# Kernel tuning notes

Hardware: AMD Instinct MI355X
Metric: run time of the kernel (lower is better)

The kernel has to match this reference:

```python
import jax, jax.numpy as jnp
import numpy as np

D_MODEL = 2048
NUM_HEADS = 16
D_HEAD = D_MODEL // NUM_HEADS


def setup_inputs() -> dict:
    key = jax.random.key(0)
    k_x, k_q, k_k, k_v, k_o, k_ob = jax.random.split(key, 6)
    B, L = 2, 2048
    s = 1.0 / np.sqrt(D_MODEL)
    return {
        "x": jax.random.normal(k_x, (B, L, D_MODEL), dtype=jnp.float32),
        # torch nn.Linear weights are (out_features, in_features)
        "Wq": jax.random.uniform(k_q, (D_MODEL, D_MODEL), jnp.float32, -s, s),
        "Wk": jax.random.uniform(k_k, (D_HEAD, D_MODEL), jnp.float32, -s, s),
        "Wv": jax.random.uniform(k_v, (D_HEAD, D_MODEL), jnp.float32, -s, s),
        "Wo": jax.random.uniform(k_o, (D_MODEL, D_MODEL), jnp.float32, -s, s),
        "bo": jax.random.uniform(k_ob, (D_MODEL,), jnp.float32, -s, s),
    }


def reference(x, Wq, Wk, Wv, Wo, bo):
    B, L, _ = x.shape
    H, dh = NUM_HEADS, D_HEAD
    Q = (x @ Wq.T).reshape(B, L, H, dh).transpose(0, 2, 1, 3)  # [B,H,L,dh]
    K = x @ Wk.T  # [B,L,dh] shared across heads (MQA)
    V = x @ Wv.T  # [B,L,dh]
    scores = jnp.einsum("bhqd,bkd->bhqk", Q, K) / np.sqrt(dh)  # [B,H,L,L]
    attn = jax.nn.softmax(scores, axis=-1)
    out = jnp.einsum("bhqk,bkd->bhqd", attn, V)  # [B,H,L,dh]
    out = out.transpose(0, 2, 1, 3).reshape(B, L, H * dh)
    return out @ Wo.T + bo
```

## Files before the change

### kernel.cpp

```cpp
#include <hip/hip_runtime.h>


typedef __attribute__((ext_vector_type(8))) short bf16x8;
typedef __attribute__((ext_vector_type(4))) short short4v;
typedef __attribute__((ext_vector_type(4))) float f32x4;
typedef __attribute__((ext_vector_type(16))) float f32x16;
typedef __attribute__((ext_vector_type(4))) int int4v;

__device__ __forceinline__ unsigned short f2bf(float f) {
  unsigned int u = __builtin_bit_cast(unsigned int, f);
  u += 0x7fffu + ((u >> 16) & 1u);
  return (unsigned short)(u >> 16);
}

__device__ __forceinline__ unsigned int cvtpk(float lo, float hi) {
  unsigned int r;
  asm("v_cvt_pk_bf16_f32 %0, %1, %2" : "=v"(r) : "v"(lo), "v"(hi));
  return r;
}

typedef __attribute__((address_space(1))) void gvoid_t;
typedef __attribute__((address_space(3))) void lvoid_t;

__device__ __forceinline__ void gll16(const void* g, void* l) {
  __builtin_amdgcn_global_load_lds((gvoid_t*)g, (lvoid_t*)l, 16, 0, 0);
}

__global__ void cast_all_kernel(
    const float* __restrict__ x, const float* __restrict__ wq,
    const float* __restrict__ wk, const float* __restrict__ wv,
    const float* __restrict__ wo, unsigned short* __restrict__ xb,
    unsigned short* __restrict__ wallb, unsigned short* __restrict__ wob) {
  const int NT = 4325376;
  int i = blockIdx.x * blockDim.x + threadIdx.x;
  const int stride = gridDim.x * blockDim.x;
  for (; i < NT; i += stride) {
    const float* src;
    unsigned short* dst;
    int j;
    if (i < 2097152) {
      src = x; dst = xb; j = i;
    } else if (i < 3145728) {
      src = wq; dst = wallb; j = i - 2097152;
    } else if (i < 3211264) {
      src = wk; dst = wallb + 2048 * 2048; j = i - 3145728;
    } else if (i < 3276800) {
      src = wv; dst = wallb + 2176 * 2048; j = i - 3211264;
    } else {
      src = wo; dst = wob; j = i - 3276800;
    }
    float4 f = reinterpret_cast<const float4*>(src)[j];
    short4v o;
    o.x = (short)f2bf(f.x);
    o.y = (short)f2bf(f.y);
    o.z = (short)f2bf(f.z);
    o.w = (short)f2bf(f.w);
    reinterpret_cast<short4v*>(dst)[j] = o;
  }
}

template <int MODE>
__global__ __launch_bounds__(256) void gemm_bt(
    const unsigned short* __restrict__ A, const unsigned short* __restrict__ B,
    void* __restrict__ Cout, int M, int N, int K, float scale,
    const float* __restrict__ bias, void* __restrict__ C2,
    void* __restrict__ C3) {
  __shared__ unsigned short As[128 * 64] __attribute__((aligned(16)));
  __shared__ unsigned short Bs[128 * 64] __attribute__((aligned(16)));

  const int tid = threadIdx.x;
  const int lane = tid & 63;
  const int wave = tid >> 6;
  const int lr = lane & 15;
  const int lg = lane >> 4;
  const int bm = blockIdx.x * 128;
  const int bn = blockIdx.y * 128;
  const int wrow = (wave >> 1) * 64;
  const int wcol = (wave & 1) * 64;

  f32x4 acc[4][4] = {};

  int soff[4];
#pragma unroll
  for (int t = 0; t < 4; t++) {
    int ci = t * 256 + tid;
    int row = ci >> 3;
    int c = (ci ^ row) & 7;
    soff[t] = row * K + c * 8;
  }
  const unsigned short* Abase = A + (size_t)bm * K;
  const unsigned short* Bbase = B + (size_t)bn * K;

  for (int k0 = 0; k0 < K; k0 += 64) {
    __syncthreads();
#pragma unroll
    for (int t = 0; t < 4; t++) {
      gll16(Abase + k0 + soff[t], (char*)As + (t * 256 + tid) * 16);
      gll16(Bbase + k0 + soff[t], (char*)Bs + (t * 256 + tid) * 16);
    }
    __syncthreads();

#pragma unroll
    for (int kh = 0; kh < 2; kh++) {
      bf16x8 af[4], bfr[4];
#pragma unroll
      for (int mi = 0; mi < 4; mi++) {
        const int row = wrow + mi * 16 + lr;
        const int ch = (lg + 4 * kh) ^ (row & 7);
        af[mi] = *(const bf16x8*)&As[row * 64 + ch * 8];
      }
#pragma unroll
      for (int nj = 0; nj < 4; nj++) {
        const int row = wcol + nj * 16 + lr;
        const int ch = (lg + 4 * kh) ^ (row & 7);
        bfr[nj] = *(const bf16x8*)&Bs[row * 64 + ch * 8];
      }
#pragma unroll
      for (int mi = 0; mi < 4; mi++)
#pragma unroll
        for (int nj = 0; nj < 4; nj++)
          acc[mi][nj] = __builtin_amdgcn_mfma_f32_16x16x32_bf16(
              af[mi], bfr[nj], acc[mi][nj], 0, 0, 0);
    }
  }

#pragma unroll
  for (int mi = 0; mi < 4; mi++)
#pragma unroll
    for (int nj = 0; nj < 4; nj++) {
      const int row = bm + wrow + mi * 16 + (lane >> 4) * 4;
      const int col = bn + wcol + nj * 16 + lr;
#pragma unroll
      for (int r = 0; r < 4; r++) {
        float v = acc[mi][nj][r];
        if constexpr (MODE == 2) {
          ((float*)Cout)[(size_t)(row + r) * N + col] = v + bias[col];
        } else {
          if (col < 2048)
            ((unsigned short*)Cout)[(size_t)(row + r) * 2048 + col] =
                f2bf(v * scale);
          else if (col < 2176)
            ((unsigned short*)C2)[(size_t)(row + r) * 128 + (col - 2048)] =
                f2bf(v);
          else
            ((unsigned short*)C3)[(size_t)(col - 2176) * M + (row + r)] =
                f2bf(v);
        }
      }
    }
}

__global__ __launch_bounds__(256, 3) void mqa_attn(
    const unsigned short* __restrict__ Q, const unsigned short* __restrict__ Kb,
    const unsigned short* __restrict__ VT, unsigned short* __restrict__ Ob) {
  __shared__ unsigned short Ksm[2][2][4096] __attribute__((aligned(16)));
  __shared__ unsigned short Vsm[2][4096] __attribute__((aligned(16)));
  __shared__ float mlbuf[2][32];

  const int tid = threadIdx.x;
  const int lane = tid & 63;
  const int wave = tid >> 6;
  const int grp = wave >> 1;
  const int wi = wave & 1;
  const int tg = tid & 127;
  const int l31 = lane & 31;
  const int hi = lane >> 5;
  const int bh = blockIdx.y;
  const int b = bh >> 4;
  const int h = bh & 15;
  const int q0 = blockIdx.x * 64 + wi * 32;
  const int kvbase = grp * 1024;

  const unsigned short* Qb = Q + ((size_t)(b * 2048 + q0)) * 2048 + h * 128;
  const unsigned short* Kbase = Kb + (size_t)b * 2048 * 128;
  const unsigned short* VTb = VT + (size_t)b * 2048;

  bf16x8 qf[8];
#pragma unroll
  for (int ks = 0; ks < 8; ks++)
    qf[ks] = *(const bf16x8*)&Qb[(size_t)l31 * 2048 + ks * 16 + hi * 8];

  f32x16 oacc[4] = {};
  float lrun = 0.0f;

  int koff[4], voff[4];
#pragma unroll
  for (int t = 0; t < 4; t++) {
    int ci = t * 128 + tg;
    int row = ci >> 4;
    int p = (ci ^ row) & 15;
    koff[t] = row * 128 + p * 8;
    voff[t] = (4 * row + (p >> 2)) * 4096 + (p & 3) * 8;
  }

  auto stageK = [&](int kv0, int bsel) {
    const unsigned short* kp = Kbase + (size_t)(kvbase + kv0) * 128;
    char* kb = (char*)&Ksm[grp][bsel][0];
#pragma unroll
    for (int t = 0; t < 4; t++) gll16(kp + koff[t], kb + (t * 128 + tg) * 16);
  };
  auto stageV = [&](int kv0) {
    const unsigned short* vp = VTb + kvbase + kv0;
    char* vb = (char*)&Vsm[grp][0];
#pragma unroll
    for (int t = 0; t < 4; t++) gll16(vp + voff[t], vb + (t * 128 + tg) * 16);
  };

  stageK(0, 0);
  stageV(0);
  asm volatile("s_waitcnt vmcnt(0)" ::: "memory");
  __builtin_amdgcn_sched_barrier(0);
  __builtin_amdgcn_s_barrier();

  for (int t = 0; t < 32; t++) {
    const int cur = t & 1;
    stageK(((t + 1) & 31) * 32, cur ^ 1);
    const unsigned short* Kt = &Ksm[grp][cur][0];
    const unsigned short* Vt = &Vsm[grp][0];

    f32x16 st = {};
#pragma unroll
    for (int ks = 0; ks < 8; ks++) {
      const int pos = (2 * ks + hi) ^ (l31 & 15);
      bf16x8 kf = *(const bf16x8*)&Kt[l31 * 128 + pos * 8];
      st = __builtin_amdgcn_mfma_f32_32x32x16_bf16(kf, qf[ks], st, 0, 0, 0);
    }

#pragma unroll
    for (int r = 0; r < 16; r++) st[r] = __builtin_amdgcn_exp2f(st[r]);
    {
      float s0 = (st[0] + st[1]) + (st[2] + st[3]);
      float s1 = (st[4] + st[5]) + (st[6] + st[7]);
      float s2 = (st[8] + st[9]) + (st[10] + st[11]);
      float s3 = (st[12] + st[13]) + (st[14] + st[15]);
      float ps = (s0 + s1) + (s2 + s3);
      lrun += ps + __shfl_xor(ps, 32);
    }

    bf16x8 paw[2];
#pragma unroll
    for (int h2 = 0; h2 < 2; h2++) {
      unsigned int a0 = cvtpk(st[8 * h2 + 0], st[8 * h2 + 1]);
      unsigned int a1 = cvtpk(st[8 * h2 + 2], st[8 * h2 + 3]);
      unsigned int b0 = cvtpk(st[8 * h2 + 4], st[8 * h2 + 5]);
      unsigned int b1 = cvtpk(st[8 * h2 + 6], st[8 * h2 + 7]);
      unsigned int s0 = hi ? a0 : b0;
      unsigned int s1 = hi ? a1 : b1;
      unsigned int r0 = (unsigned int)__shfl_xor((int)s0, 32);
      unsigned int r1 = (unsigned int)__shfl_xor((int)s1, 32);
      int4v w;
      w.x = (int)(hi ? r0 : a0);
      w.y = (int)(hi ? r1 : a1);
      w.z = (int)(hi ? b0 : r0);
      w.w = (int)(hi ? b1 : r1);
      paw[h2] = __builtin_bit_cast(bf16x8, w);
    }

    asm volatile("s_waitcnt vmcnt(4)" ::: "memory");
    __builtin_amdgcn_sched_barrier(0);
    __builtin_amdgcn_s_barrier();

#pragma unroll
    for (int dt = 0; dt < 4; dt++) {
      f32x16 z = oacc[dt];
      const int qr = dt * 8 + (l31 >> 2);
#pragma unroll
      for (int ks2 = 0; ks2 < 2; ks2++) {
        const int pos = (4 * (l31 & 3) + 2 * ks2 + hi) ^ (qr & 15);
        bf16x8 vfr = *(const bf16x8*)&Vt[qr * 128 + pos * 8];
        z = __builtin_amdgcn_mfma_f32_32x32x16_bf16(paw[ks2], vfr, z, 0, 0, 0);
      }
      oacc[dt] = z;
    }

    __builtin_amdgcn_s_barrier();
    stageV(((t + 1) & 31) * 32);
    asm volatile("s_waitcnt vmcnt(4)" ::: "memory");
    __builtin_amdgcn_sched_barrier(0);
    __builtin_amdgcn_s_barrier();
  }

  float* mg = (float*)&Ksm[0][0][0] + (size_t)wi * 4096;
  if (grp == 1) {
#pragma unroll
    for (int dt = 0; dt < 4; dt++)
#pragma unroll
      for (int r = 0; r < 16; r++)
        mg[(dt * 16 + r) * 64 + lane] = oacc[dt][r];
    if (hi == 0) mlbuf[wi][l31] = lrun;
  }
  __syncthreads();
  if (grp == 0) {
    float lb = mlbuf[wi][l31];
    float linv = 1.0f / (lrun + lb);
#pragma unroll
    for (int r = 0; r < 16; r++) {
      const int qrow = (r & 3) + 8 * (r >> 2) + 4 * hi;
      float invr = __shfl(linv, qrow);
      size_t row = (size_t)(b * 2048 + q0 + qrow);
#pragma unroll
      for (int dt = 0; dt < 4; dt++) {
        float o = (oacc[dt][r] + mg[(dt * 16 + r) * 64 + lane]) * invr;
        Ob[row * 2048 + h * 128 + dt * 32 + l31] = f2bf(o);
      }
    }
  }
}

extern "C" void kernel_launch(void* const* d_in, const int* in_sizes, int n_in,
                              void* d_out, int out_size, void* d_ws,
                              size_t ws_size, hipStream_t stream) {
  const float* x = (const float*)d_in[0];
  const float* Wq = (const float*)d_in[1];
  const float* Wk = (const float*)d_in[2];
  const float* Wv = (const float*)d_in[3];
  const float* Wo = (const float*)d_in[4];
  const float* bo = (const float*)d_in[5];

  const int Bb = 2, Lq = 2048, D = 2048, DH = 128;
  const int M = Bb * Lq;

  char* ws = (char*)d_ws;
  size_t off = 0;
  auto alloc = [&](size_t bytes) {
    void* p = ws + off;
    off += (bytes + 255) & ~size_t(255);
    return p;
  };
  unsigned short* x_bf = (unsigned short*)alloc((size_t)M * D * 2);
  unsigned short* Wall_bf = (unsigned short*)alloc((size_t)2304 * D * 2);
  unsigned short* Wo_bf = (unsigned short*)alloc((size_t)D * D * 2);
  unsigned short* Qbuf = (unsigned short*)alloc((size_t)M * D * 2);
  unsigned short* Kbuf = (unsigned short*)alloc((size_t)M * DH * 2);
  unsigned short* VTbuf = (unsigned short*)alloc((size_t)DH * M * 2);
  unsigned short* AObuf = (unsigned short*)alloc((size_t)M * D * 2);

  cast_all_kernel<<<2048, 256, 0, stream>>>(x, Wq, Wk, Wv, Wo, x_bf, Wall_bf,
                                            Wo_bf);

  gemm_bt<4><<<dim3(M / 128, 2304 / 128), 256, 0, stream>>>(
      x_bf, Wall_bf, Qbuf, M, 2304, D, 0.12752041986f, nullptr, Kbuf, VTbuf);
  mqa_attn<<<dim3(Lq / 64, Bb * 16), 256, 0, stream>>>(Qbuf, Kbuf, VTbuf,
                                                       AObuf);
  gemm_bt<2><<<dim3(M / 128, D / 128), 256, 0, stream>>>(
      AObuf, Wo_bf, d_out, M, D, D, 1.0f, bo, nullptr, nullptr);
}
```

Before: 222.8 us.

## Drop KV split in attention; each block handles 128 queries over full KV

The attention kernel previously split each 64-query block's KV range across two wave groups and merged partial outputs and row sums through shared memory at the end. Now all four waves cover distinct 32-query slices, so each block handles 128 queries over the full KV range. K and V tiles are 64 keys wide and shared by all four waves. This doubles reuse of staged K/V per block, removes the final cross-group merge and the syncthreads, and halves the grid. In exchange, the block count drops to 512, the loop carries twice the score registers, and the sequential KV loop per wave is twice as long.

```diff
diff --git a/kernel.cpp b/kernel.cpp
--- a/kernel.cpp
+++ b/kernel.cpp
@@ -153,23 +153,18 @@
 __global__ __launch_bounds__(256, 3) void mqa_attn(
     const unsigned short* __restrict__ Q, const unsigned short* __restrict__ Kb,
     const unsigned short* __restrict__ VT, unsigned short* __restrict__ Ob) {
-  __shared__ unsigned short Ksm[2][2][4096] __attribute__((aligned(16)));
-  __shared__ unsigned short Vsm[2][4096] __attribute__((aligned(16)));
-  __shared__ float mlbuf[2][32];
+  __shared__ unsigned short Ksm[2][8192] __attribute__((aligned(16)));
+  __shared__ unsigned short Vsm[8192] __attribute__((aligned(16)));
 
   const int tid = threadIdx.x;
   const int lane = tid & 63;
-  const int wave = tid >> 6;
-  const int grp = wave >> 1;
-  const int wi = wave & 1;
-  const int tg = tid & 127;
+  const int wi = tid >> 6;
   const int l31 = lane & 31;
   const int hi = lane >> 5;
   const int bh = blockIdx.y;
   const int b = bh >> 4;
   const int h = bh & 15;
-  const int q0 = blockIdx.x * 64 + wi * 32;
-  const int kvbase = grp * 1024;
+  const int q0 = blockIdx.x * 128 + wi * 32;
 
   const unsigned short* Qb = Q + ((size_t)(b * 2048 + q0)) * 2048 + h * 128;
   const unsigned short* Kbase = Kb + (size_t)b * 2048 * 128;
@@ -186,24 +181,24 @@
   int koff[4], voff[4];
 #pragma unroll
   for (int t = 0; t < 4; t++) {
-    int ci = t * 128 + tg;
+    int ci = t * 256 + tid;
     int row = ci >> 4;
     int p = (ci ^ row) & 15;
     koff[t] = row * 128 + p * 8;
-    voff[t] = (4 * row + (p >> 2)) * 4096 + (p & 3) * 8;
+    voff[t] = (2 * row + (p >> 3)) * 4096 + (p & 7) * 8;
   }
 
   auto stageK = [&](int kv0, int bsel) {
-    const unsigned short* kp = Kbase + (size_t)(kvbase + kv0) * 128;
-    char* kb = (char*)&Ksm[grp][bsel][0];
-#pragma unroll
-    for (int t = 0; t < 4; t++) gll16(kp + koff[t], kb + (t * 128 + tg) * 16);
+    const unsigned short* kp = Kbase + (size_t)kv0 * 128;
+    char* kb = (char*)&Ksm[bsel][0];
+#pragma unroll
+    for (int t = 0; t < 4; t++) gll16(kp + koff[t], kb + (t * 256 + tid) * 16);
   };
   auto stageV = [&](int kv0) {
-    const unsigned short* vp = VTb + kvbase + kv0;
-    char* vb = (char*)&Vsm[grp][0];
-#pragma unroll
-    for (int t = 0; t < 4; t++) gll16(vp + voff[t], vb + (t * 128 + tg) * 16);
+    const unsigned short* vp = VTb + kv0;
+    char* vb = (char*)&Vsm[0];
+#pragma unroll
+    for (int t = 0; t < 4; t++) gll16(vp + voff[t], vb + (t * 256 + tid) * 16);
   };
 
   stageK(0, 0);
@@ -214,47 +209,61 @@
 
   for (int t = 0; t < 32; t++) {
     const int cur = t & 1;
-    stageK(((t + 1) & 31) * 32, cur ^ 1);
-    const unsigned short* Kt = &Ksm[grp][cur][0];
-    const unsigned short* Vt = &Vsm[grp][0];
-
-    f32x16 st = {};
+    stageK(((t + 1) & 31) * 64, cur ^ 1);
+    const unsigned short* Kt = &Ksm[cur][0];
+    const unsigned short* Vt = &Vsm[0];
+
+    f32x16 st[2] = {};
 #pragma unroll
     for (int ks = 0; ks < 8; ks++) {
-      const int pos = (2 * ks + hi) ^ (l31 & 15);
-      bf16x8 kf = *(const bf16x8*)&Kt[l31 * 128 + pos * 8];
-      st = __builtin_amdgcn_mfma_f32_32x32x16_bf16(kf, qf[ks], st, 0, 0, 0);
-    }
-
-#pragma unroll
-    for (int r = 0; r < 16; r++) st[r] = __builtin_amdgcn_exp2f(st[r]);
+#pragma unroll
+      for (int sub = 0; sub < 2; sub++) {
+        const int krow = sub * 32 + l31;
+        const int pos = (2 * ks + hi) ^ (krow & 15);
+        bf16x8 kf = *(const bf16x8*)&Kt[krow * 128 + pos * 8];
+        st[sub] =
+            __builtin_amdgcn_mfma_f32_32x32x16_bf16(kf, qf[ks], st[sub], 0, 0, 0);
+      }
+    }
+
+#pragma unroll
+    for (int sub = 0; sub < 2; sub++)
+#pragma unroll
+      for (int r = 0; r < 16; r++)
+        st[sub][r] = __builtin_amdgcn_exp2f(st[sub][r]);
     {
-      float s0 = (st[0] + st[1]) + (st[2] + st[3]);
-      float s1 = (st[4] + st[5]) + (st[6] + st[7]);
-      float s2 = (st[8] + st[9]) + (st[10] + st[11]);
-      float s3 = (st[12] + st[13]) + (st[14] + st[15]);
-      float ps = (s0 + s1) + (s2 + s3);
+      float s0 = (st[0][0] + st[0][1]) + (st[0][2] + st[0][3]);
+      float s1 = (st[0][4] + st[0][5]) + (st[0][6] + st[0][7]);
+      float s2 = (st[0][8] + st[0][9]) + (st[0][10] + st[0][11]);
+      float s3 = (st[0][12] + st[0][13]) + (st[0][14] + st[0][15]);
+      float s4 = (st[1][0] + st[1][1]) + (st[1][2] + st[1][3]);
+      float s5 = (st[1][4] + st[1][5]) + (st[1][6] + st[1][7]);
+      float s6 = (st[1][8] + st[1][9]) + (st[1][10] + st[1][11]);
+      float s7 = (st[1][12] + st[1][13]) + (st[1][14] + st[1][15]);
+      float ps = ((s0 + s1) + (s2 + s3)) + ((s4 + s5) + (s6 + s7));
       lrun += ps + __shfl_xor(ps, 32);
     }
 
-    bf16x8 paw[2];
-#pragma unroll
-    for (int h2 = 0; h2 < 2; h2++) {
-      unsigned int a0 = cvtpk(st[8 * h2 + 0], st[8 * h2 + 1]);
-      unsigned int a1 = cvtpk(st[8 * h2 + 2], st[8 * h2 + 3]);
-      unsigned int b0 = cvtpk(st[8 * h2 + 4], st[8 * h2 + 5]);
-      unsigned int b1 = cvtpk(st[8 * h2 + 6], st[8 * h2 + 7]);
-      unsigned int s0 = hi ? a0 : b0;
-      unsigned int s1 = hi ? a1 : b1;
-      unsigned int r0 = (unsigned int)__shfl_xor((int)s0, 32);
-      unsigned int r1 = (unsigned int)__shfl_xor((int)s1, 32);
-      int4v w;
-      w.x = (int)(hi ? r0 : a0);
-      w.y = (int)(hi ? r1 : a1);
-      w.z = (int)(hi ? b0 : r0);
-      w.w = (int)(hi ? b1 : r1);
-      paw[h2] = __builtin_bit_cast(bf16x8, w);
-    }
+    bf16x8 paw[4];
+#pragma unroll
+    for (int sub = 0; sub < 2; sub++)
+#pragma unroll
+      for (int h2 = 0; h2 < 2; h2++) {
+        unsigned int a0 = cvtpk(st[sub][8 * h2 + 0], st[sub][8 * h2 + 1]);
+        unsigned int a1 = cvtpk(st[sub][8 * h2 + 2], st[sub][8 * h2 + 3]);
+        unsigned int b0 = cvtpk(st[sub][8 * h2 + 4], st[sub][8 * h2 + 5]);
+        unsigned int b1 = cvtpk(st[sub][8 * h2 + 6], st[sub][8 * h2 + 7]);
+        unsigned int s0 = hi ? a0 : b0;
+        unsigned int s1 = hi ? a1 : b1;
+        unsigned int r0 = (unsigned int)__shfl_xor((int)s0, 32);
+        unsigned int r1 = (unsigned int)__shfl_xor((int)s1, 32);
+        int4v w;
+        w.x = (int)(hi ? r0 : a0);
+        w.y = (int)(hi ? r1 : a1);
+        w.z = (int)(hi ? b0 : r0);
+        w.w = (int)(hi ? b1 : r1);
+        paw[sub * 2 + h2] = __builtin_bit_cast(bf16x8, w);
+      }
 
     asm volatile("s_waitcnt vmcnt(4)" ::: "memory");
     __builtin_amdgcn_sched_barrier(0);
@@ -263,47 +272,32 @@
 #pragma unroll
     for (int dt = 0; dt < 4; dt++) {
       f32x16 z = oacc[dt];
-      const int qr = dt * 8 + (l31 >> 2);
-#pragma unroll
-      for (int ks2 = 0; ks2 < 2; ks2++) {
-        const int pos = (4 * (l31 & 3) + 2 * ks2 + hi) ^ (qr & 15);
-        bf16x8 vfr = *(const bf16x8*)&Vt[qr * 128 + pos * 8];
+      const int s = dt * 16 + (l31 >> 1);
+#pragma unroll
+      for (int ks2 = 0; ks2 < 4; ks2++) {
+        const int pos = (8 * (l31 & 1) + 2 * ks2 + hi) ^ (s & 15);
+        bf16x8 vfr = *(const bf16x8*)&Vt[s * 128 + pos * 8];
         z = __builtin_amdgcn_mfma_f32_32x32x16_bf16(paw[ks2], vfr, z, 0, 0, 0);
       }
       oacc[dt] = z;
     }
 
     __builtin_amdgcn_s_barrier();
-    stageV(((t + 1) & 31) * 32);
+    stageV(((t + 1) & 31) * 64);
     asm volatile("s_waitcnt vmcnt(4)" ::: "memory");
     __builtin_amdgcn_sched_barrier(0);
     __builtin_amdgcn_s_barrier();
   }
 
-  float* mg = (float*)&Ksm[0][0][0] + (size_t)wi * 4096;
-  if (grp == 1) {
+  float linv = 1.0f / lrun;
+#pragma unroll
+  for (int r = 0; r < 16; r++) {
+    const int qrow = (r & 3) + 8 * (r >> 2) + 4 * hi;
+    float invr = __shfl(linv, qrow);
+    size_t row = (size_t)(b * 2048 + q0 + qrow);
 #pragma unroll
     for (int dt = 0; dt < 4; dt++)
-#pragma unroll
-      for (int r = 0; r < 16; r++)
-        mg[(dt * 16 + r) * 64 + lane] = oacc[dt][r];
-    if (hi == 0) mlbuf[wi][l31] = lrun;
-  }
-  __syncthreads();
-  if (grp == 0) {
-    float lb = mlbuf[wi][l31];
-    float linv = 1.0f / (lrun + lb);
-#pragma unroll
-    for (int r = 0; r < 16; r++) {
-      const int qrow = (r & 3) + 8 * (r >> 2) + 4 * hi;
-      float invr = __shfl(linv, qrow);
-      size_t row = (size_t)(b * 2048 + q0 + qrow);
-#pragma unroll
-      for (int dt = 0; dt < 4; dt++) {
-        float o = (oacc[dt][r] + mg[(dt * 16 + r) * 64 + lane]) * invr;
-        Ob[row * 2048 + h * 128 + dt * 32 + l31] = f2bf(o);
-      }
-    }
+      Ob[row * 2048 + h * 128 + dt * 32 + l31] = f2bf(oacc[dt][r] * invr);
   }
 }
 
@@ -340,8 +334,8 @@
 
   gemm_bt<4><<<dim3(M / 128, 2304 / 128), 256, 0, stream>>>(
       x_bf, Wall_bf, Qbuf, M, 2304, D, 0.12752041986f, nullptr, Kbuf, VTbuf);
-  mqa_attn<<<dim3(Lq / 64, Bb * 16), 256, 0, stream>>>(Qbuf, Kbuf, VTbuf,
-                                                       AObuf);
+  mqa_attn<<<dim3(Lq / 128, Bb * 16), 256, 0, stream>>>(Qbuf, Kbuf, VTbuf,
+                                                        AObuf);
   gemm_bt<2><<<dim3(M / 128, D / 128), 256, 0, stream>>>(
       AObuf, Wo_bf, d_out, M, D, D, 1.0f, bo, nullptr, nullptr);
 }
```

Result: faster. 198.3 us, median of 2 (-11.0%).
